# Kernel optimization log

Hardware: AMD Instinct MI355X
Metric: run time of the kernel (lower is better)

## Reference

```python
import jax, jax.numpy as jnp
import numpy as np

B, S, D, H, DK = 2, 2048, 1024, 16, 64
NUM_BUCKETS, MAX_DIST = 32, 128
EPS = 1e-6


def _relative_position_bucket(rel, num_buckets=NUM_BUCKETS, max_distance=MAX_DIST):
    # bidirectional (T5 encoder) bucketing
    nb = num_buckets // 2
    bucket = (rel > 0).astype(jnp.int32) * nb
    n = jnp.abs(rel)
    max_exact = nb // 2
    is_small = n < max_exact
    large = max_exact + (
        jnp.log(jnp.maximum(n, 1).astype(jnp.float32) / max_exact)
        / np.log(max_distance / max_exact)
        * (nb - max_exact)
    ).astype(jnp.int32)
    large = jnp.minimum(large, nb - 1)
    return bucket + jnp.where(is_small, n, large)


def softmax1(logits):
    # off-by-one softmax: exp(x-m) / (sum(exp(x-m)) + exp(-m))
    m = jax.lax.stop_gradient(jnp.max(logits, axis=-1, keepdims=True))
    e = jnp.exp(logits - m)
    return e / (jnp.sum(e, axis=-1, keepdims=True) + jnp.exp(-m))


def setup_inputs() -> dict:
    key = jax.random.key(0)
    ks = jax.random.split(key, 8)
    scale = 0.02
    return {
        "hidden_states": jax.random.normal(ks[0], (B, S, D), dtype=jnp.float32),
        "delete_gate_mask": jax.random.normal(ks[1], (B, S, 1), dtype=jnp.float32),
        "ln_w": jnp.ones((D,), dtype=jnp.float32),
        "q_w": jax.random.normal(ks[2], (D, H * DK), dtype=jnp.float32) * scale,
        "k_w": jax.random.normal(ks[3], (D, H * DK), dtype=jnp.float32) * scale,
        "v_w": jax.random.normal(ks[4], (D, H * DK), dtype=jnp.float32) * scale,
        "o_w": jax.random.normal(ks[5], (H * DK, D), dtype=jnp.float32) * scale,
        "rel_emb": jax.random.normal(ks[6], (NUM_BUCKETS, H), dtype=jnp.float32) * scale,
    }


def reference(hidden_states, delete_gate_mask, ln_w, q_w, k_w, v_w, o_w, rel_emb):
    # T5LayerNorm (RMS norm, no mean subtraction, no bias)
    var = jnp.mean(jnp.square(hidden_states), axis=-1, keepdims=True)
    x = hidden_states * jax.lax.rsqrt(var + EPS) * ln_w

    # projections (T5 Linear layers have no bias, no 1/sqrt(d) scaling)
    q = (x @ q_w).reshape(B, S, H, DK).transpose(0, 2, 1, 3)  # bhqd
    k = (x @ k_w).reshape(B, S, H, DK).transpose(0, 2, 1, 3)  # bhkd
    v = (x @ v_w).reshape(B, S, H, DK).transpose(0, 2, 1, 3)  # bhkd

    scores = jnp.einsum("bhqd,bhkd->bhqk", q, k)

    # relative position bias: [1, H, S, S]
    pos = jnp.arange(S)
    rel = pos[None, :] - pos[:, None]  # key_pos - query_pos
    bucket = _relative_position_bucket(rel)  # [S, S]
    position_bias = rel_emb[bucket].transpose(2, 0, 1)[None]  # [1,H,S,S]

    # delete gate: [B,S,1] -> additive mask over key axis [B,1,1,S]
    gate = delete_gate_mask[..., 0][:, None, None, :]

    scores = scores + position_bias + gate
    attn = softmax1(scores.astype(jnp.float32)).astype(scores.dtype)

    attn_out = jnp.einsum("bhqk,bhkd->bhqd", attn, v)
    attn_out = attn_out.transpose(0, 2, 1, 3).reshape(B, S, H * DK) @ o_w

    # residual (dropout disabled at p=0)
    return hidden_states + attn_out
```

## Files before the change

kernel.cpp:

```cpp
#include <hip/hip_runtime.h>
#include <hip/hip_bf16.h>
#include <math.h>

typedef __attribute__((ext_vector_type(8))) short short8;
typedef __attribute__((ext_vector_type(4))) float f32x4;

#define S_LEN   2048
#define DMODEL  1024
#define NHEAD   16
#define HDK     64
#define NBATCH  2
#define MTOT    (NBATCH*S_LEN)
#define LOG2E   1.4426950408889634f

__device__ __forceinline__ unsigned short f2bf(float f) {
  union { float f; unsigned u; } c; c.f = f;
  unsigned r = c.u + 0x7FFFu + ((c.u >> 16) & 1u);
  return (unsigned short)(r >> 16);
}

__device__ __forceinline__ short8 lds_ld16(const unsigned short* p) {
  return *reinterpret_cast<const short8*>(p);
}

__device__ __forceinline__ void gload_lds16(const unsigned short* g, unsigned short* l) {
  __builtin_amdgcn_global_load_lds(
      (const __attribute__((address_space(1))) unsigned int*)g,
      (__attribute__((address_space(3))) unsigned int*)l, 16, 0, 0);
}

__global__ __launch_bounds__(256) void transpose_w_kernel(
    const float* __restrict__ qw, const float* __restrict__ kw,
    const float* __restrict__ vw, const float* __restrict__ ow,
    unsigned short* __restrict__ wqkv, unsigned short* __restrict__ wo) {
  int z = blockIdx.z;
  const float* src = (z==0)?qw:(z==1)?kw:(z==2)?vw:ow;
  unsigned short* dst = (z<3) ? (wqkv + (size_t)z*DMODEL*DMODEL) : wo;
  __shared__ float tile[32][33];
  int n0 = blockIdx.x*32, k0 = blockIdx.y*32;
  int tx = threadIdx.x, ty = threadIdx.y;
  for (int r = ty; r < 32; r += 8)
    tile[r][tx] = src[(size_t)(k0+r)*DMODEL + n0 + tx];
  __syncthreads();
  for (int r = ty; r < 32; r += 8)
    dst[(size_t)(n0+r)*DMODEL + k0 + tx] = f2bf(tile[tx][r]);
}

__global__ void bias_table_kernel(const float* __restrict__ rel_emb,
                                  float* __restrict__ btab) {
  int idx = blockIdx.x*256 + threadIdx.x;
  if (idx >= NHEAD*4095) return;
  int h = idx / 4095, rp = idx % 4095, rel = rp - 2047;
  int bucket = (rel > 0) ? 16 : 0;
  int n = (rel < 0) ? -rel : rel;
  int v;
  if (n < 8) v = n;
  else {
    float lrv = logf((float)n * 0.125f) / 2.7725887f * 8.0f;
    v = 8 + (int)lrv;
    if (v > 15) v = 15;
  }
  btab[idx] = rel_emb[(size_t)(bucket + v)*NHEAD + h] * LOG2E;
}

__global__ __launch_bounds__(256) void rmsnorm_kernel(
    const float* __restrict__ hs, const float* __restrict__ lnw,
    unsigned short* __restrict__ xo) {
  int row = blockIdx.x, t = threadIdx.x;
  const float4 v = ((const float4*)(hs + (size_t)row*DMODEL))[t];
  float ss = v.x*v.x + v.y*v.y + v.z*v.z + v.w*v.w;
  #pragma unroll
  for (int off = 32; off >= 1; off >>= 1) ss += __shfl_xor(ss, off, 64);
  __shared__ float wsum[4];
  if ((t & 63) == 0) wsum[t >> 6] = ss;
  __syncthreads();
  float tot = wsum[0] + wsum[1] + wsum[2] + wsum[3];
  float sc = rsqrtf(tot * (1.0f/DMODEL) + 1e-6f);
  const float4 lw = ((const float4*)lnw)[t];
  uint2 o;
  o.x = (unsigned)f2bf(v.x*sc*lw.x) | ((unsigned)f2bf(v.y*sc*lw.y) << 16);
  o.y = (unsigned)f2bf(v.z*sc*lw.z) | ((unsigned)f2bf(v.w*sc*lw.w) << 16);
  ((uint2*)(xo + (size_t)row*DMODEL))[t] = o;
}

template<int EPI>
__global__ __launch_bounds__(256) void gemm128(
    const unsigned short* __restrict__ A,
    const unsigned short* __restrict__ Bt,
    unsigned short* __restrict__ Oq, unsigned short* __restrict__ Ok,
    unsigned short* __restrict__ Ov,
    const float* __restrict__ resid, float* __restrict__ Of) {
  __shared__ unsigned short As[128*32];
  __shared__ unsigned short Bs[128*32];
  const int m0 = blockIdx.x*128, n0 = blockIdx.y*128;
  const unsigned short* Bz = Bt + ((EPI==0) ? (size_t)blockIdx.z*DMODEL*DMODEL : 0);
  const int t = threadIdx.x, lane = t & 63, w = t >> 6;
  const int g = lane >> 4, lr = lane & 15;
  const int wr = (w >> 1)*64, wc = (w & 1)*64;

  f32x4 acc[4][4];
  #pragma unroll
  for (int mi = 0; mi < 4; mi++)
    #pragma unroll
    for (int ni = 0; ni < 4; ni++) acc[mi][ni] = (f32x4){0.f,0.f,0.f,0.f};

  const int i0 = t, i1 = t + 256;
  const unsigned short* a0 = A  + (size_t)(m0 + (i0>>2))*DMODEL + (i0&3)*8;
  const unsigned short* a1 = A  + (size_t)(m0 + (i1>>2))*DMODEL + (i1&3)*8;
  const unsigned short* b0 = Bz + (size_t)(n0 + (i0>>2))*DMODEL + (i0&3)*8;
  const unsigned short* b1 = Bz + (size_t)(n0 + (i1>>2))*DMODEL + (i1&3)*8;
  unsigned short* lA0 = As + i0*8;
  unsigned short* lA1 = As + i1*8;
  unsigned short* lB0 = Bs + i0*8;
  unsigned short* lB1 = Bs + i1*8;

  for (int kk = 0; kk < DMODEL; kk += 32) {
    gload_lds16(a0 + kk, lA0);
    gload_lds16(a1 + kk, lA1);
    gload_lds16(b0 + kk, lB0);
    gload_lds16(b1 + kk, lB1);
    __syncthreads();
    short8 af[4], bfr[4];
    #pragma unroll
    for (int mi = 0; mi < 4; mi++) af[mi]  = lds_ld16(As + (wr + mi*16 + lr)*32 + g*8);
    #pragma unroll
    for (int ni = 0; ni < 4; ni++) bfr[ni] = lds_ld16(Bs + (wc + ni*16 + lr)*32 + g*8);
    #pragma unroll
    for (int mi = 0; mi < 4; mi++)
      #pragma unroll
      for (int ni = 0; ni < 4; ni++)
        acc[mi][ni] = __builtin_amdgcn_mfma_f32_16x16x32_bf16(af[mi], bfr[ni], acc[mi][ni], 0, 0, 0);
    __syncthreads();
  }

  if (EPI == 0) {
    unsigned short* dst = (blockIdx.z == 0) ? Oq : Ok;
    const float osc = (blockIdx.z == 0) ? LOG2E : 1.0f;
    #pragma unroll
    for (int mi = 0; mi < 4; mi++) {
      #pragma unroll
      for (int r = 0; r < 4; r++) {
        int m = m0 + wr + mi*16 + g*4 + r;
        int b = m >> 11, s = m & (S_LEN-1);
        unsigned short* drow = dst + ((size_t)b*NHEAD*S_LEN + s)*HDK;
        #pragma unroll
        for (int ni = 0; ni < 4; ni++) {
          int n = n0 + wc + ni*16 + lr;
          int h = n >> 6, dcol = n & 63;
          drow[(size_t)h*S_LEN*HDK + dcol] = f2bf(acc[mi][ni][r] * osc);
        }
      }
    }
  } else if (EPI == 2) {
    #pragma unroll
    for (int ni = 0; ni < 4; ni++) {
      int n = n0 + wc + ni*16 + lr;
      int b = n >> 11, s = n & (S_LEN-1);
      #pragma unroll
      for (int mi = 0; mi < 4; mi++)
        #pragma unroll
        for (int r = 0; r < 4; r++) {
          int m = m0 + wr + mi*16 + g*4 + r;
          Ov[((size_t)b*DMODEL + m)*S_LEN + s] = f2bf(acc[mi][ni][r]);
        }
    }
  } else {
    #pragma unroll
    for (int mi = 0; mi < 4; mi++) {
      #pragma unroll
      for (int r = 0; r < 4; r++) {
        int m = m0 + wr + mi*16 + g*4 + r;
        const float* rrow = resid + (size_t)m*DMODEL;
        float* orow = Of + (size_t)m*DMODEL;
        #pragma unroll
        for (int ni = 0; ni < 4; ni++) {
          int n = n0 + wc + ni*16 + lr;
          orow[n] = rrow[n] + acc[mi][ni][r];
        }
      }
    }
  }
}

__global__ __launch_bounds__(256, 2) void attn_kernel(
    const unsigned short* __restrict__ Qg,
    const unsigned short* __restrict__ Kg,
    const unsigned short* __restrict__ Vtg,
    const float* __restrict__ btab,
    const float* __restrict__ gmask,
    unsigned short* __restrict__ Og) {
  __shared__ __align__(16) unsigned short Kl[2][64][64];
  __shared__ __align__(16) unsigned short Vl[2][64][64];
  __shared__ __align__(16) unsigned short Pl[4][16*64];
  __shared__ __align__(16) float gl[S_LEN];

  const int bh = blockIdx.y, b = bh >> 4, h = bh & 15;
  const int q0 = blockIdx.x * 128;
  const int t = threadIdx.x, w = t >> 6, lane = t & 63;
  const int g = lane >> 4, lr = lane & 15, l7 = lane & 7;
  const int srow0 = t >> 3, sg0 = t & 7, srow1 = srow0 + 32;
  const int swz = (sg0 ^ (srow0 & 7)) << 3;

  const unsigned short* Qb = Qg  + (size_t)bh*S_LEN*HDK;
  const unsigned short* Kb = Kg  + (size_t)bh*S_LEN*HDK;
  const unsigned short* Vb = Vtg + (size_t)bh*HDK*S_LEN;

  {
    const float4* gm4 = (const float4*)(gmask + (size_t)b*S_LEN);
    #pragma unroll
    for (int i = 0; i < 2; i++) {
      int idx = t + i*256;
      float4 gv = gm4[idx];
      float4 gs; gs.x = gv.x*LOG2E; gs.y = gv.y*LOG2E; gs.z = gv.z*LOG2E; gs.w = gv.w*LOG2E;
      ((float4*)gl)[idx] = gs;
    }
  }

  const int qs0A = q0 + w*32, qs0B = qs0A + 16;
  short8 qfA0 = *reinterpret_cast<const short8*>(Qb + (size_t)(qs0A+lr)*HDK + g*8);
  short8 qfA1 = *reinterpret_cast<const short8*>(Qb + (size_t)(qs0A+lr)*HDK + 32 + g*8);
  short8 qfB0 = *reinterpret_cast<const short8*>(Qb + (size_t)(qs0B+lr)*HDK + g*8);
  short8 qfB1 = *reinterpret_cast<const short8*>(Qb + (size_t)(qs0B+lr)*HDK + 32 + g*8);

  f32x4 accA[4], accB[4];
  #pragma unroll
  for (int n = 0; n < 4; n++) { accA[n] = (f32x4){0.f,0.f,0.f,0.f}; accB[n] = (f32x4){0.f,0.f,0.f,0.f}; }
  float mA = -1e30f, lA = 0.f, mB = -1e30f, lB = 0.f;

  const float* btb = btab + (size_t)h*4095 + 2047;
  const float cpos = btb[91];
  const float cneg = btb[-91];

  {
    *reinterpret_cast<uint4*>(&Kl[0][srow0][swz]) =
        *reinterpret_cast<const uint4*>(Kb + (size_t)srow0*HDK + sg0*8);
    *reinterpret_cast<uint4*>(&Kl[0][srow1][swz]) =
        *reinterpret_cast<const uint4*>(Kb + (size_t)srow1*HDK + sg0*8);
    *reinterpret_cast<uint4*>(&Vl[0][srow0][swz]) =
        *reinterpret_cast<const uint4*>(Vb + (size_t)srow0*S_LEN + sg0*8);
    *reinterpret_cast<uint4*>(&Vl[0][srow1][swz]) =
        *reinterpret_cast<const uint4*>(Vb + (size_t)srow1*S_LEN + sg0*8);
  }

  char* prow = (char*)&Pl[w][0] + lr*128;

  int cur = 0;
  const int NT = S_LEN/64;
  for (int kt = 0; kt < NT; ++kt) {
    const int key0 = kt*64;
    __syncthreads();

    uint4 nk0, nk1, nv0, nv1;
    const bool pf = (kt + 1 < NT);
    if (pf) {
      nk0 = *reinterpret_cast<const uint4*>(Kb + (size_t)(key0+64+srow0)*HDK + sg0*8);
      nk1 = *reinterpret_cast<const uint4*>(Kb + (size_t)(key0+64+srow1)*HDK + sg0*8);
      nv0 = *reinterpret_cast<const uint4*>(Vb + (size_t)srow0*S_LEN + key0+64 + sg0*8);
      nv1 = *reinterpret_cast<const uint4*>(Vb + (size_t)srow1*S_LEN + key0+64 + sg0*8);
    }

    short8 bk[4][2];
    #pragma unroll
    for (int n = 0; n < 4; n++) {
      const unsigned short* kr = &Kl[cur][n*16 + lr][0];
      bk[n][0] = lds_ld16(kr + ((g ^ l7) << 3));
      bk[n][1] = lds_ld16(kr + (((4 + g) ^ l7) << 3));
    }
    short8 bv[2][4];
    #pragma unroll
    for (int c = 0; c < 2; c++)
      #pragma unroll
      for (int n = 0; n < 4; n++)
        bv[c][n] = lds_ld16(&Vl[cur][n*16 + lr][((4*c + g) ^ l7) << 3]);
    float4 gq[4];
    #pragma unroll
    for (int n = 0; n < 4; n++) gq[n] = *(const float4*)&gl[key0 + n*16 + g*4];

    f32x4 svA[4], svB[4];
    #pragma unroll
    for (int n = 0; n < 4; n++) {
      f32x4 z = (f32x4){0.f,0.f,0.f,0.f};
      svA[n] = __builtin_amdgcn_mfma_f32_16x16x32_bf16(bk[n][0], qfA0, z, 0, 0, 0);
      svA[n] = __builtin_amdgcn_mfma_f32_16x16x32_bf16(bk[n][1], qfA1, svA[n], 0, 0, 0);
      svB[n] = __builtin_amdgcn_mfma_f32_16x16x32_bf16(bk[n][0], qfB0, z, 0, 0, 0);
      svB[n] = __builtin_amdgcn_mfma_f32_16x16x32_bf16(bk[n][1], qfB1, svB[n], 0, 0, 0);
    }

#define PROCESS_SET(sv_, m_, l_, acc_, qs0_)                                          \
    {                                                                                 \
      float s_[4][4];                                                                 \
      _Pragma("unroll") for (int n = 0; n < 4; n++)                                   \
        _Pragma("unroll") for (int r = 0; r < 4; r++) s_[n][r] = sv_[n][r];           \
      const int dband = key0 - (qs0_);                                                \
      if (dband > -154 && dband < 106) {                                              \
        const float* btq = btb + (dband - lr);                                        \
        _Pragma("unroll") for (int n = 0; n < 4; n++)                                 \
          _Pragma("unroll") for (int r = 0; r < 4; r++)                               \
            s_[n][r] += gq[n][r] + btq[n*16 + g*4 + r];                               \
      } else {                                                                        \
        const float cc = (dband > 0) ? cpos : cneg;                                   \
        _Pragma("unroll") for (int n = 0; n < 4; n++)                                 \
          _Pragma("unroll") for (int r = 0; r < 4; r++)                               \
            s_[n][r] += gq[n][r] + cc;                                                \
      }                                                                               \
      float pmax = s_[0][0];                                                          \
      _Pragma("unroll") for (int n = 0; n < 4; n++)                                   \
        _Pragma("unroll") for (int r = 0; r < 4; r++) pmax = fmaxf(pmax, s_[n][r]);   \
      if (__any(pmax > m_ + 8.0f)) {                                                  \
        float tm = pmax;                                                              \
        tm = fmaxf(tm, __shfl_xor(tm, 16));                                           \
        tm = fmaxf(tm, __shfl_xor(tm, 32));                                           \
        float mnew = fmaxf(m_, tm);                                                   \
        float scv = exp2f(m_ - mnew);                                                 \
        m_ = mnew; l_ *= scv;                                                         \
        _Pragma("unroll") for (int r = 0; r < 4; r++) {                               \
          float s4 = __shfl(scv, g*4 + r, 16);                                        \
          _Pragma("unroll") for (int n = 0; n < 4; n++) acc_[n][r] *= s4;             \
        }                                                                             \
      }                                                                               \
      _Pragma("unroll") for (int n = 0; n < 4; n++)                                   \
        _Pragma("unroll") for (int r = 0; r < 4; r++) {                               \
          float p = exp2f(s_[n][r] - m_);                                             \
          s_[n][r] = p; l_ += p;                                                      \
        }                                                                             \
      _Pragma("unroll") for (int n = 0; n < 4; n++) {                                 \
        unsigned plo_, phi_;                                                          \
        asm("v_cvt_pk_bf16_f32 %0, %1, %2" : "=v"(plo_) : "v"(s_[n][0]), "v"(s_[n][1])); \
        asm("v_cvt_pk_bf16_f32 %0, %1, %2" : "=v"(phi_) : "v"(s_[n][2]), "v"(s_[n][3])); \
        uint2 pw_; pw_.x = plo_; pw_.y = phi_;                                        \
        *reinterpret_cast<uint2*>(prow + ((((2*n + (g>>1)) ^ l7) << 4) + ((g & 1) << 3))) = pw_; \
      }                                                                               \
      _Pragma("unroll") for (int c = 0; c < 2; c++) {                                 \
        short8 pa_ = lds_ld16((const unsigned short*)(prow + (((4*c + g) ^ l7) << 4))); \
        _Pragma("unroll") for (int n = 0; n < 4; n++)                                 \
          acc_[n] = __builtin_amdgcn_mfma_f32_16x16x32_bf16(pa_, bv[c][n], acc_[n], 0, 0, 0); \
      }                                                                               \
    }

    PROCESS_SET(svA, mA, lA, accA, qs0A)
    PROCESS_SET(svB, mB, lB, accB, qs0B)
#undef PROCESS_SET

    if (pf) {
      *reinterpret_cast<uint4*>(&Kl[cur^1][srow0][swz]) = nk0;
      *reinterpret_cast<uint4*>(&Kl[cur^1][srow1][swz]) = nk1;
      *reinterpret_cast<uint4*>(&Vl[cur^1][srow0][swz]) = nv0;
      *reinterpret_cast<uint4*>(&Vl[cur^1][srow1][swz]) = nv1;
    }
    cur ^= 1;
  }

#define FINAL_SET(m_, l_, acc_, qs0_)                                                 \
  {                                                                                   \
    float rs = l_;                                                                    \
    rs += __shfl_xor(rs, 16);                                                         \
    rs += __shfl_xor(rs, 32);                                                         \
    float inv = 1.0f / (rs + exp2f(-m_));                                             \
    _Pragma("unroll") for (int r = 0; r < 4; r++) {                                   \
      float inv4 = __shfl(inv, g*4 + r, 16);                                          \
      int srw = (qs0_) + g*4 + r;                                                     \
      unsigned short* orow = Og + ((size_t)b*S_LEN + srw)*DMODEL + h*HDK;             \
      _Pragma("unroll") for (int n = 0; n < 4; n++)                                   \
        orow[n*16 + lr] = f2bf(acc_[n][r] * inv4);                                    \
    }                                                                                 \
  }
  FINAL_SET(mA, lA, accA, qs0A)
  FINAL_SET(mB, lB, accB, qs0B)
#undef FINAL_SET
}

extern "C" void kernel_launch(void* const* d_in, const int* in_sizes, int n_in,
                              void* d_out, int out_size, void* d_ws, size_t ws_size,
                              hipStream_t stream) {
  const float* hs   = (const float*)d_in[0];
  const float* gate = (const float*)d_in[1];
  const float* lnw  = (const float*)d_in[2];
  const float* qw   = (const float*)d_in[3];
  const float* kw   = (const float*)d_in[4];
  const float* vw   = (const float*)d_in[5];
  const float* ow   = (const float*)d_in[6];
  const float* rel  = (const float*)d_in[7];
  float* out = (float*)d_out;

  char* ws = (char*)d_ws;
  const size_t MB = 1ull << 20;
  unsigned short* xbf  = (unsigned short*)(ws);
  unsigned short* wqkv = (unsigned short*)(ws + 8*MB);
  unsigned short* wo   = (unsigned short*)(ws + 14*MB);
  unsigned short* qb   = (unsigned short*)(ws + 16*MB);
  unsigned short* kb   = (unsigned short*)(ws + 24*MB);
  unsigned short* vt   = (unsigned short*)(ws + 32*MB);
  unsigned short* ao   = (unsigned short*)(ws + 40*MB);
  float*          btab = (float*)(ws + 48*MB);

  transpose_w_kernel<<<dim3(32,32,4), dim3(32,8), 0, stream>>>(qw, kw, vw, ow, wqkv, wo);
  bias_table_kernel<<<dim3(256), dim3(256), 0, stream>>>(rel, btab);
  rmsnorm_kernel<<<dim3(MTOT), dim3(256), 0, stream>>>(hs, lnw, xbf);
  gemm128<0><<<dim3(MTOT/128, DMODEL/128, 2), dim3(256), 0, stream>>>(
      xbf, wqkv, qb, kb, nullptr, nullptr, nullptr);
  gemm128<2><<<dim3(DMODEL/128, MTOT/128, 1), dim3(256), 0, stream>>>(
      wqkv + (size_t)2*DMODEL*DMODEL, xbf, nullptr, nullptr, vt, nullptr, nullptr);
  attn_kernel<<<dim3(S_LEN/128, NBATCH*NHEAD), dim3(256), 0, stream>>>(
      qb, kb, vt, btab, gate, ao);
  gemm128<1><<<dim3(MTOT/128, DMODEL/128, 1), dim3(256), 0, stream>>>(
      ao, wo, nullptr, nullptr, nullptr, hs, out);
}
```

Measured before the change: 163.2 us.

## Deepen GEMM K-tile with swizzled LDS, remap attention grid per XCD, add MFMA priority

The GEMM K-step grows from 32 to 64, with an XOR-swizzled LDS layout so fragment reads avoid bank conflicts and the loop runs half as many barriers. The attention launch becomes a flat 1D grid remapped so each XCD handles the q-blocks of a few heads together, aiming for better L2 reuse of K and V. s_setprio calls raise wave priority around the MFMA sections to improve overlap with softmax work in other waves. Doubling the GEMM LDS footprint may reduce occupancy.

```diff
diff --git a/kernel.cpp b/kernel.cpp
--- a/kernel.cpp
+++ b/kernel.cpp
@@ -90,8 +90,8 @@
     unsigned short* __restrict__ Oq, unsigned short* __restrict__ Ok,
     unsigned short* __restrict__ Ov,
     const float* __restrict__ resid, float* __restrict__ Of) {
-  __shared__ unsigned short As[128*32];
-  __shared__ unsigned short Bs[128*32];
+  __shared__ unsigned short As[128*64];
+  __shared__ unsigned short Bs[128*64];
   const int m0 = blockIdx.x*128, n0 = blockIdx.y*128;
   const unsigned short* Bz = Bt + ((EPI==0) ? (size_t)blockIdx.z*DMODEL*DMODEL : 0);
   const int t = threadIdx.x, lane = t & 63, w = t >> 6;
@@ -104,32 +104,44 @@
     #pragma unroll
     for (int ni = 0; ni < 4; ni++) acc[mi][ni] = (f32x4){0.f,0.f,0.f,0.f};
 
-  const int i0 = t, i1 = t + 256;
-  const unsigned short* a0 = A  + (size_t)(m0 + (i0>>2))*DMODEL + (i0&3)*8;
-  const unsigned short* a1 = A  + (size_t)(m0 + (i1>>2))*DMODEL + (i1&3)*8;
-  const unsigned short* b0 = Bz + (size_t)(n0 + (i0>>2))*DMODEL + (i0&3)*8;
-  const unsigned short* b1 = Bz + (size_t)(n0 + (i1>>2))*DMODEL + (i1&3)*8;
-  unsigned short* lA0 = As + i0*8;
-  unsigned short* lA1 = As + i1*8;
-  unsigned short* lB0 = Bs + i0*8;
-  unsigned short* lB1 = Bs + i1*8;
-
-  for (int kk = 0; kk < DMODEL; kk += 32) {
-    gload_lds16(a0 + kk, lA0);
-    gload_lds16(a1 + kk, lA1);
-    gload_lds16(b0 + kk, lB0);
-    gload_lds16(b1 + kk, lB1);
+  const unsigned short* ag[4]; const unsigned short* bg[4];
+  unsigned short* al[4]; unsigned short* bl[4];
+  #pragma unroll
+  for (int i = 0; i < 4; i++) {
+    int slot = t + i*256, row = slot >> 3, c8 = slot & 7;
+    int cs = c8 ^ (row & 7);
+    ag[i] = A  + (size_t)(m0 + row)*DMODEL + cs*8;
+    bg[i] = Bz + (size_t)(n0 + row)*DMODEL + cs*8;
+    al[i] = As + slot*8;
+    bl[i] = Bs + slot*8;
+  }
+
+  for (int kk = 0; kk < DMODEL; kk += 64) {
+    #pragma unroll
+    for (int i = 0; i < 4; i++) {
+      gload_lds16(ag[i] + kk, al[i]);
+      gload_lds16(bg[i] + kk, bl[i]);
+    }
     __syncthreads();
-    short8 af[4], bfr[4];
-    #pragma unroll
-    for (int mi = 0; mi < 4; mi++) af[mi]  = lds_ld16(As + (wr + mi*16 + lr)*32 + g*8);
-    #pragma unroll
-    for (int ni = 0; ni < 4; ni++) bfr[ni] = lds_ld16(Bs + (wc + ni*16 + lr)*32 + g*8);
-    #pragma unroll
-    for (int mi = 0; mi < 4; mi++)
-      #pragma unroll
-      for (int ni = 0; ni < 4; ni++)
-        acc[mi][ni] = __builtin_amdgcn_mfma_f32_16x16x32_bf16(af[mi], bfr[ni], acc[mi][ni], 0, 0, 0);
+    #pragma unroll
+    for (int ks = 0; ks < 2; ks++) {
+      short8 af[4], bfr[4];
+      #pragma unroll
+      for (int mi = 0; mi < 4; mi++) {
+        int R = wr + mi*16 + lr;
+        af[mi] = lds_ld16(As + R*64 + (((ks*4 + g) ^ (R & 7)) << 3));
+      }
+      #pragma unroll
+      for (int ni = 0; ni < 4; ni++) {
+        int R = wc + ni*16 + lr;
+        bfr[ni] = lds_ld16(Bs + R*64 + (((ks*4 + g) ^ (R & 7)) << 3));
+      }
+      #pragma unroll
+      for (int mi = 0; mi < 4; mi++)
+        #pragma unroll
+        for (int ni = 0; ni < 4; ni++)
+          acc[mi][ni] = __builtin_amdgcn_mfma_f32_16x16x32_bf16(af[mi], bfr[ni], acc[mi][ni], 0, 0, 0);
+    }
     __syncthreads();
   }
 
@@ -194,8 +206,12 @@
   __shared__ __align__(16) unsigned short Pl[4][16*64];
   __shared__ __align__(16) float gl[S_LEN];
 
-  const int bh = blockIdx.y, b = bh >> 4, h = bh & 15;
-  const int q0 = blockIdx.x * 128;
+  const int flat = blockIdx.x;
+  const int xcd = flat & 7, j = flat >> 3;
+  const int bh = xcd*4 + (j >> 4), qx = j & 15;
+  const int b = bh >> 4, h = bh & 15;
+  const int q0 = qx * 128;
+
   const int t = threadIdx.x, w = t >> 6, lane = t & 63;
   const int g = lane >> 4, lr = lane & 15, l7 = lane & 7;
   const int srow0 = t >> 3, sg0 = t & 7, srow1 = srow0 + 32;
@@ -277,6 +293,7 @@
     for (int n = 0; n < 4; n++) gq[n] = *(const float4*)&gl[key0 + n*16 + g*4];
 
     f32x4 svA[4], svB[4];
+    __builtin_amdgcn_s_setprio(1);
     #pragma unroll
     for (int n = 0; n < 4; n++) {
       f32x4 z = (f32x4){0.f,0.f,0.f,0.f};
@@ -285,6 +302,7 @@
       svB[n] = __builtin_amdgcn_mfma_f32_16x16x32_bf16(bk[n][0], qfB0, z, 0, 0, 0);
       svB[n] = __builtin_amdgcn_mfma_f32_16x16x32_bf16(bk[n][1], qfB1, svB[n], 0, 0, 0);
     }
+    __builtin_amdgcn_s_setprio(0);
 
 #define PROCESS_SET(sv_, m_, l_, acc_, qs0_)                                          \
     {                                                                                 \
@@ -330,11 +348,13 @@
         uint2 pw_; pw_.x = plo_; pw_.y = phi_;                                        \
         *reinterpret_cast<uint2*>(prow + ((((2*n + (g>>1)) ^ l7) << 4) + ((g & 1) << 3))) = pw_; \
       }                                                                               \
+      __builtin_amdgcn_s_setprio(1);                                                  \
       _Pragma("unroll") for (int c = 0; c < 2; c++) {                                 \
         short8 pa_ = lds_ld16((const unsigned short*)(prow + (((4*c + g) ^ l7) << 4))); \
         _Pragma("unroll") for (int n = 0; n < 4; n++)                                 \
           acc_[n] = __builtin_amdgcn_mfma_f32_16x16x32_bf16(pa_, bv[c][n], acc_[n], 0, 0, 0); \
       }                                                                               \
+      __builtin_amdgcn_s_setprio(0);                                                  \
     }
 
     PROCESS_SET(svA, mA, lA, accA, qs0A)
@@ -400,7 +420,7 @@
       xbf, wqkv, qb, kb, nullptr, nullptr, nullptr);
   gemm128<2><<<dim3(DMODEL/128, MTOT/128, 1), dim3(256), 0, stream>>>(
       wqkv + (size_t)2*DMODEL*DMODEL, xbf, nullptr, nullptr, vt, nullptr, nullptr);
-  attn_kernel<<<dim3(S_LEN/128, NBATCH*NHEAD), dim3(256), 0, stream>>>(
+  attn_kernel<<<dim3(512), dim3(256), 0, stream>>>(
       qb, kb, vt, btab, gate, ao);
   gemm128<1><<<dim3(MTOT/128, DMODEL/128, 1), dim3(256), 0, stream>>>(
       ao, wo, nullptr, nullptr, nullptr, hs, out);
```

New measurement: 154.7 us. 1.05x faster.
